# Performance work log

Hardware: AMD Instinct MI355X
Metric: run time of the kernel (lower is better)

Reference implementation:

```python
import jax, jax.numpy as jnp
import numpy as np

BETA = 0.25  # commitment cost (original code's undefined self.betas)


def setup_inputs() -> dict:
    key = jax.random.key(0)
    k1, k2 = jax.random.split(key)
    B, D, H, W = 32, 256, 32, 32
    K = 1024
    x = jax.random.normal(k1, (B, D, H, W), dtype=jnp.float32)
    # nn.Embedding init: uniform(-1/K, 1/K)
    emb = jax.random.uniform(k2, (K, D), dtype=jnp.float32,
                             minval=-1.0 / K, maxval=1.0 / K)
    return {"x": x, "emb": emb}


def reference(x, emb):
    # x: [B, D, H, W] -> NHWC
    xp = jnp.transpose(x, (0, 2, 3, 1))          # [B, H, W, D]
    D = emb.shape[1]
    z = xp.reshape(-1, D)                        # [N, D]
    # pairwise squared distance: ||z||^2 + ||e||^2 - 2 z e^T
    dist = (jnp.sum(z * z, axis=1, keepdims=True)
            + jnp.sum(emb * emb, axis=1)
            - 2.0 * jnp.einsum('nd,kd->nk', z, emb))  # [N, K]
    idx = jnp.argmin(dist, axis=1)               # [N] int
    z_quant = emb[idx].reshape(xp.shape)         # [B, H, W, D]
    sg = jax.lax.stop_gradient
    loss = (jnp.mean((sg(z_quant) - xp) ** 2)
            + BETA * jnp.mean((z_quant - sg(xp)) ** 2))
    # straight-through estimator
    z_quant = xp + sg(z_quant - xp)
    z_quant = jnp.transpose(z_quant, (0, 3, 1, 2))  # back to NCHW
    return z_quant, idx, loss
```

## Files before the change

kernel.cpp:

```cpp
#include <hip/hip_runtime.h>

typedef _Float16 half8 __attribute__((ext_vector_type(8)));
typedef _Float16 half4v __attribute__((ext_vector_type(4)));
typedef float f32x4 __attribute__((ext_vector_type(4)));

#define ZQ_ELEMS 8388608
#define N_TOK    32768
#define D_DIM    256
#define K_CB     1024

#define FLAG_CAP 8192
#define ESCALE   1024.0f
#define TAU      0.15f

__device__ __align__(16) _Float16 g_eh[K_CB * D_DIM];
__device__ __align__(16) float g_ebT[D_DIM * K_CB];
__device__ float g_ck[K_CB];
__device__ float g_bk[K_CB];
__device__ float g_loss;
__device__ int   g_cnt;
__device__ int   g_flags[FLAG_CAP];
__device__ float g_zst[FLAG_CAP * 256];
__device__ float g_aA[FLAG_CAP];
__device__ unsigned long long g_best[FLAG_CAP];

__device__ __forceinline__ unsigned long long enc_dk(float D, int k) {
  unsigned int b = __float_as_uint(D);
  unsigned int u = (b & 0x80000000u) ? ~b : (b | 0x80000000u);
  return (((unsigned long long)u) << 32) | (unsigned int)k;
}

__global__ __launch_bounds__(256) void vq_prep(const float* __restrict__ emb) {
  __shared__ float tl[64][65];
  const int tid = threadIdx.x;
  const int w   = tid >> 6;
  const int l   = tid & 63;
  const int k   = (blockIdx.x << 2) + w;
  f32x4 v = *(const f32x4*)(emb + (k << 8) + (l << 2));
  double sd = (double)v[0]*v[0] + (double)v[1]*v[1] + (double)v[2]*v[2] + (double)v[3]*v[3];
  #pragma unroll
  for (int m = 1; m < 64; m <<= 1) sd += __shfl_xor(sd, m);
  if (l == 0) { g_bk[k] = (float)sd; g_ck[k] = 512.0f * (float)sd; }
  half4v h;
  h[0] = (_Float16)(v[0] * ESCALE); h[1] = (_Float16)(v[1] * ESCALE);
  h[2] = (_Float16)(v[2] * ESCALE); h[3] = (_Float16)(v[3] * ESCALE);
  *(half4v*)(g_eh + (k << 8) + (l << 2)) = h;
  const int gi = blockIdx.x * 256 + tid;
  if (gi < FLAG_CAP) g_best[gi] = ~0ULL;
  if (blockIdx.x == 0 && tid == 0) { g_loss = 0.0f; g_cnt = 0; }
  if (blockIdx.x < 64) {
    const int tx = tid & 63, ty = tid >> 6;
    const int k0 = (blockIdx.x & 15) << 6;
    const int d0 = (blockIdx.x >> 4) << 6;
    #pragma unroll
    for (int j = 0; j < 16; j++) {
      const int kk = (ty << 4) + j;
      tl[kk][tx] = emb[((k0 + kk) << 8) + d0 + tx];
    }
    __syncthreads();
    #pragma unroll
    for (int j = 0; j < 16; j++) {
      const int dd = (ty << 4) + j;
      g_ebT[((d0 + dd) << 10) + k0 + tx] = tl[tx][dd];
    }
  }
}

__global__ __launch_bounds__(256, 4) void vq_main(const float* __restrict__ x,
                                                  const float* __restrict__ emb,
                                                  float* __restrict__ out) {
  __shared__ __align__(16) _Float16 zt[32 * 256];
  __shared__ float ckl[K_CB];
  __shared__ float wv1[4][32], wv2[4][32];
  __shared__ int   wi1[4][32];
  __shared__ int   fidx[32];
  __shared__ float lred[4];
  __shared__ int   fcnt;
  __shared__ int   fslot[32], ftok[32];

  const int tid = threadIdx.x;
  const int n0  = blockIdx.x << 5;
  const int b   = blockIdx.x >> 5;
  const int hw0 = (blockIdx.x & 31) << 5;

  if (tid == 0) fcnt = 0;

  #pragma unroll
  for (int i = 0; i < 4; i++) ckl[tid + 256 * i] = g_ck[tid + 256 * i];

  {
    const int hw8 = (tid & 3) << 3;
    const int dl  = tid >> 2;
    #pragma unroll
    for (int it = 0; it < 4; it++) {
      const int d = (it << 6) + dl;
      const float* src = x + (((b << 8) + d) << 10) + hw0 + hw8;
      f32x4 a0 = *(const f32x4*)src;
      f32x4 a1 = *(const f32x4*)(src + 4);
      _Float16 cv[8];
      cv[0]=(_Float16)a0[0]; cv[1]=(_Float16)a0[1]; cv[2]=(_Float16)a0[2]; cv[3]=(_Float16)a0[3];
      cv[4]=(_Float16)a1[0]; cv[5]=(_Float16)a1[1]; cv[6]=(_Float16)a1[2]; cv[7]=(_Float16)a1[3];
      const int blkx = d >> 3;
      #pragma unroll
      for (int i = 0; i < 8; i++) {
        const int n   = hw8 + i;
        const int blk = blkx ^ i ^ (tid & 3);
        zt[(n << 8) + (blk << 3) + (d & 7)] = cv[i];
      }
    }
  }
  __syncthreads();

  const int w = tid >> 6;
  const int l = tid & 63;
  const int c = l & 15;
  const int q = l >> 4;

  half8 af[2][8];
  #pragma unroll
  for (int t = 0; t < 2; t++) {
    const int n  = (t << 4) + c;
    const int sw = (n & 7) ^ (n >> 3);
    #pragma unroll
    for (int s = 0; s < 8; s++) {
      const int K = (s << 2) + q;
      af[t][s] = *(const half8*)(zt + (n << 8) + ((K ^ sw) << 3));
    }
  }

  float v1[2][4], v2[2][4]; int i1[2][4];
  #pragma unroll
  for (int t = 0; t < 2; t++)
    #pragma unroll
    for (int r = 0; r < 4; r++) { v1[t][r] = -3e38f; v2[t][r] = -3e38f; i1[t][r] = 0; }

  for (int jj = 0; jj < 16; jj++) {
    const int k0 = (w << 4) + (jj << 6);
    const float ckv = ckl[k0 + c];
    f32x4 acc[2];
    acc[0] = f32x4{-ckv, -ckv, -ckv, -ckv};
    acc[1] = f32x4{-ckv, -ckv, -ckv, -ckv};
    #pragma unroll
    for (int s = 0; s < 8; s++) {
      const half8 bf = *(const half8*)(g_eh + ((k0 + c) << 8) + (s << 5) + (q << 3));
      acc[0] = __builtin_amdgcn_mfma_f32_16x16x32_f16(af[0][s], bf, acc[0], 0, 0, 0);
      acc[1] = __builtin_amdgcn_mfma_f32_16x16x32_f16(af[1][s], bf, acc[1], 0, 0, 0);
    }
    const int kk = k0 + c;
    #pragma unroll
    for (int t = 0; t < 2; t++)
      #pragma unroll
      for (int r = 0; r < 4; r++) {
        const float sv = acc[t][r];
        if (sv > v1[t][r]) { v2[t][r] = v1[t][r]; v1[t][r] = sv; i1[t][r] = kk; }
        else if (sv > v2[t][r]) v2[t][r] = sv;
      }
  }

  #pragma unroll
  for (int t = 0; t < 2; t++)
    #pragma unroll
    for (int r = 0; r < 4; r++) {
      float a1v = v1[t][r], a2v = v2[t][r]; int ai = i1[t][r];
      #pragma unroll
      for (int m = 8; m >= 1; m >>= 1) {
        const float o1 = __shfl_xor(a1v, m);
        const int   oi = __shfl_xor(ai, m);
        const float o2 = __shfl_xor(a2v, m);
        if (o1 > a1v || (o1 == a1v && oi < ai)) { a2v = fmaxf(a1v, o2); a1v = o1; ai = oi; }
        else a2v = fmaxf(a2v, o1);
      }
      if (c == 0) {
        const int nl = (t << 4) + (q << 2) + r;
        wv1[w][nl] = a1v; wv2[w][nl] = a2v; wi1[w][nl] = ai;
      }
    }
  __syncthreads();

  if (tid < 32) {
    float a1v = wv1[0][tid], a2v = wv2[0][tid]; int ai = wi1[0][tid];
    #pragma unroll
    for (int ww = 1; ww < 4; ww++) {
      const float o1 = wv1[ww][tid]; const int oi = wi1[ww][tid]; const float o2 = wv2[ww][tid];
      if (o1 > a1v || (o1 == a1v && oi < ai)) { a2v = fmaxf(a1v, o2); a1v = o1; ai = oi; }
      else a2v = fmaxf(a2v, o1);
    }
    fidx[tid] = ai;
    out[ZQ_ELEMS + n0 + tid] = (float)ai;
    if (a1v - a2v < TAU) {
      int p = atomicAdd(&g_cnt, 1);
      if (p < FLAG_CAP) {
        g_flags[p] = n0 + tid;
        int lp = atomicAdd(&fcnt, 1);
        fslot[lp] = p; ftok[lp] = n0 + tid;
      }
    }
  }
  __syncthreads();

  float lacc = 0.0f;
  {
    const int hw = tid & 31;
    const int g  = tid >> 5;
    const int sw = (hw & 7) ^ (hw >> 3);
    const float* erow = emb + (fidx[hw] << 8);
    #pragma unroll
    for (int it = 0; it < 4; it++) {
      const int dblk = (it << 3) + g;
      half8 zv = *(const half8*)(zt + (hw << 8) + ((dblk ^ sw) << 3));
      f32x4 e0 = *(const f32x4*)(erow + (dblk << 3));
      f32x4 e1 = *(const f32x4*)(erow + (dblk << 3) + 4);
      #pragma unroll
      for (int j = 0; j < 8; j++) {
        const int d = (dblk << 3) + j;
        const float ef = (j < 4) ? e0[j] : e1[j - 4];
        const float df = ef - (float)zv[j];
        lacc += df * df;
        out[(((b << 8) + d) << 10) + hw0 + hw] = ef;
      }
    }
  }
  #pragma unroll
  for (int m = 1; m < 64; m <<= 1) lacc += __shfl_xor(lacc, m);
  if (l == 0) lred[w] = lacc;
  __syncthreads();
  if (tid == 0) atomicAdd(&g_loss, lred[0] + lred[1] + lred[2] + lred[3]);

  const int nf = fcnt;
  for (int f = 0; f < nf; f++) {
    const int s = fslot[f];
    const int n = ftok[f];
    const int bb = n >> 10, hw = n & 1023;
    const float zv = x[(((bb << 8) + tid) << 10) + hw];
    g_zst[(s << 8) + tid] = zv;
    ckl[tid] = zv;
    __syncthreads();
    if (tid < 32) {
      double sa = 0.0;
      #pragma unroll
      for (int j = 0; j < 8; j++) { const double z = (double)ckl[(tid << 3) + j]; sa += z * z; }
      #pragma unroll
      for (int m = 1; m < 32; m <<= 1) sa += __shfl_xor(sa, m);
      if (tid == 0) g_aA[s] = (float)sa;
    }
    __syncthreads();
  }
}

__global__ __launch_bounds__(256) void vq_fix() {
  __shared__ float z0l[256], z1l[256];
  __shared__ float bvv[2][256];
  __shared__ int   bkk[2][256];
  const int tid = threadIdx.x;
  int cnt = g_cnt; if (cnt > FLAG_CAP) cnt = FLAG_CAP;
  const int njob = ((cnt + 1) >> 1) << 2;
  for (int j = blockIdx.x; j < njob; j += gridDim.x) {
    const int pr = j >> 2, r = j & 3;
    const int s0 = pr << 1;
    const int s1 = (s0 + 1 < cnt) ? s0 + 1 : cnt - 1;
    z0l[tid] = g_zst[(s0 << 8) + tid];
    z1l[tid] = g_zst[(s1 << 8) + tid];
    __syncthreads();
    double c0 = 0.0, c1 = 0.0;
    const float* colbase = g_ebT + (r << 8) + tid;
    #pragma unroll 8
    for (int d = 0; d < 256; d++) {
      const double e = (double)colbase[d << 10];
      c0 = fma(e, (double)z0l[d], c0);
      c1 = fma(e, (double)z1l[d], c1);
    }
    const int k = (r << 8) + tid;
    const float bkv = g_bk[k];
    bvv[0][tid] = (g_aA[s0] + bkv) - 2.0f * (float)c0;
    bkk[0][tid] = k;
    bvv[1][tid] = (g_aA[s1] + bkv) - 2.0f * (float)c1;
    bkk[1][tid] = k;
    __syncthreads();
    for (int off = 128; off >= 1; off >>= 1) {
      if (tid < off) {
        #pragma unroll
        for (int g = 0; g < 2; g++) {
          const float v2c = bvv[g][tid + off]; const int k2 = bkk[g][tid + off];
          if (v2c < bvv[g][tid] || (v2c == bvv[g][tid] && k2 < bkk[g][tid])) {
            bvv[g][tid] = v2c; bkk[g][tid] = k2;
          }
        }
      }
      __syncthreads();
    }
    if (tid == 0) {
      atomicMin(&g_best[s0], enc_dk(bvv[0][0], bkk[0][0]));
      atomicMin(&g_best[s1], enc_dk(bvv[1][0], bkk[1][0]));
    }
    __syncthreads();
  }
}

__global__ __launch_bounds__(256) void vq_out(const float* __restrict__ emb,
                                              float* __restrict__ out) {
  const int tid = threadIdx.x;
  if (blockIdx.x == 0 && tid == 0)
    out[ZQ_ELEMS + N_TOK] = g_loss * (1.25f / 8388608.0f);
  int cnt = g_cnt; if (cnt > FLAG_CAP) cnt = FLAG_CAP;
  for (int s = blockIdx.x; s < cnt; s += gridDim.x) {
    const int n = g_flags[s];
    const int kw = (int)(unsigned int)(g_best[s] & 0xFFFFFFFFu);
    const int kold = (int)out[ZQ_ELEMS + n];
    __syncthreads();
    if (tid == 0) out[ZQ_ELEMS + n] = (float)kw;
    if (kw != kold) {
      const int bb = n >> 10, hw = n & 1023;
      out[(((bb << 8) + tid) << 10) + hw] = emb[(kw << 8) + tid];
    }
  }
}

extern "C" void kernel_launch(void* const* d_in, const int* in_sizes, int n_in,
                              void* d_out, int out_size, void* d_ws, size_t ws_size,
                              hipStream_t stream) {
  const float* x   = (const float*)d_in[0];
  const float* emb = (const float*)d_in[1];
  float* out = (float*)d_out;
  vq_prep<<<256, 256, 0, stream>>>(emb);
  vq_main<<<1024, 256, 0, stream>>>(x, emb, out);
  vq_fix<<<1536, 256, 0, stream>>>();
  vq_out<<<256, 256, 0, stream>>>(emb, out);
}
```

Baseline: 225.0 us.

## Double tokens per main block, batch four tokens in fix, fuse output kernel

The main kernel now uses 512-thread blocks that each handle 64 tokens. Each wave computes two codebook column tiles per step against four token tiles, with the A fragments read from LDS on every step instead of held in registers. The fix kernel processes four flagged tokens per job, which reuses each codebook column load across more tokens. The former output kernel is folded into the last fix block, selected by an atomic completion counter, which saves a launch. The risk is that one block now does all of the output scatter serially, and the main kernel has fewer blocks and possibly more register pressure.

```diff
diff --git a/kernel.cpp b/kernel.cpp
--- a/kernel.cpp
+++ b/kernel.cpp
@@ -12,6 +12,7 @@
 #define FLAG_CAP 8192
 #define ESCALE   1024.0f
 #define TAU      0.15f
+#define FIX_GRID 768
 
 __device__ __align__(16) _Float16 g_eh[K_CB * D_DIM];
 __device__ __align__(16) float g_ebT[D_DIM * K_CB];
@@ -19,6 +20,7 @@
 __device__ float g_bk[K_CB];
 __device__ float g_loss;
 __device__ int   g_cnt;
+__device__ int   g_fixdone;
 __device__ int   g_flags[FLAG_CAP];
 __device__ float g_zst[FLAG_CAP * 256];
 __device__ float g_aA[FLAG_CAP];
@@ -47,7 +49,7 @@
   *(half4v*)(g_eh + (k << 8) + (l << 2)) = h;
   const int gi = blockIdx.x * 256 + tid;
   if (gi < FLAG_CAP) g_best[gi] = ~0ULL;
-  if (blockIdx.x == 0 && tid == 0) { g_loss = 0.0f; g_cnt = 0; }
+  if (blockIdx.x == 0 && tid == 0) { g_loss = 0.0f; g_cnt = 0; g_fixdone = 0; }
   if (blockIdx.x < 64) {
     const int tx = tid & 63, ty = tid >> 6;
     const int k0 = (blockIdx.x & 15) << 6;
@@ -66,31 +68,30 @@
   }
 }
 
-__global__ __launch_bounds__(256, 4) void vq_main(const float* __restrict__ x,
+__global__ __launch_bounds__(512, 4) void vq_main(const float* __restrict__ x,
                                                   const float* __restrict__ emb,
                                                   float* __restrict__ out) {
-  __shared__ __align__(16) _Float16 zt[32 * 256];
+  __shared__ __align__(16) _Float16 zt[64 * 256];
   __shared__ float ckl[K_CB];
-  __shared__ float wv1[4][32], wv2[4][32];
-  __shared__ int   wi1[4][32];
-  __shared__ int   fidx[32];
-  __shared__ float lred[4];
+  __shared__ float wv1[8][64], wv2[8][64];
+  __shared__ int   wi1[8][64];
+  __shared__ int   fidx[64];
+  __shared__ float lred[8];
   __shared__ int   fcnt;
-  __shared__ int   fslot[32], ftok[32];
+  __shared__ int   fslot[64], ftok[64];
 
   const int tid = threadIdx.x;
-  const int n0  = blockIdx.x << 5;
-  const int b   = blockIdx.x >> 5;
-  const int hw0 = (blockIdx.x & 31) << 5;
+  const int n0  = blockIdx.x << 6;
+  const int b   = blockIdx.x >> 4;
+  const int hw0 = (blockIdx.x & 15) << 6;
 
   if (tid == 0) fcnt = 0;
-
-  #pragma unroll
-  for (int i = 0; i < 4; i++) ckl[tid + 256 * i] = g_ck[tid + 256 * i];
+  ckl[tid] = g_ck[tid];
+  ckl[tid + 512] = g_ck[tid + 512];
 
   {
-    const int hw8 = (tid & 3) << 3;
-    const int dl  = tid >> 2;
+    const int hw8 = (tid & 7) << 3;
+    const int dl  = tid >> 3;
     #pragma unroll
     for (int it = 0; it < 4; it++) {
       const int d = (it << 6) + dl;
@@ -104,7 +105,7 @@
       #pragma unroll
       for (int i = 0; i < 8; i++) {
         const int n   = hw8 + i;
-        const int blk = blkx ^ i ^ (tid & 3);
+        const int blk = blkx ^ i ^ (tid & 7);
         zt[(n << 8) + (blk << 3) + (d & 7)] = cv[i];
       }
     }
@@ -116,49 +117,52 @@
   const int c = l & 15;
   const int q = l >> 4;
 
-  half8 af[2][8];
+  float v1[4][4], v2[4][4]; int i1[4][4];
   #pragma unroll
-  for (int t = 0; t < 2; t++) {
-    const int n  = (t << 4) + c;
-    const int sw = (n & 7) ^ (n >> 3);
+  for (int t = 0; t < 4; t++)
+    #pragma unroll
+    for (int r = 0; r < 4; r++) { v1[t][r] = -3e38f; v2[t][r] = -3e38f; i1[t][r] = 0; }
+
+  for (int jj = 0; jj < 4; jj++) {
+    const int k0  = (w << 5) + (jj << 8);
+    const int kk0 = k0 + c;
+    const int kk1 = kk0 + 16;
+    const float ckv0 = ckl[kk0];
+    const float ckv1 = ckl[kk1];
+    f32x4 acc0[4], acc1[4];
+    #pragma unroll
+    for (int t = 0; t < 4; t++) {
+      acc0[t] = f32x4{-ckv0, -ckv0, -ckv0, -ckv0};
+      acc1[t] = f32x4{-ckv1, -ckv1, -ckv1, -ckv1};
+    }
     #pragma unroll
     for (int s = 0; s < 8; s++) {
-      const int K = (s << 2) + q;
-      af[t][s] = *(const half8*)(zt + (n << 8) + ((K ^ sw) << 3));
-    }
-  }
-
-  float v1[2][4], v2[2][4]; int i1[2][4];
+      const half8 bf0 = *(const half8*)(g_eh + (kk0 << 8) + (s << 5) + (q << 3));
+      const half8 bf1 = *(const half8*)(g_eh + (kk1 << 8) + (s << 5) + (q << 3));
+      #pragma unroll
+      for (int t = 0; t < 4; t++) {
+        const int n  = (t << 4) + c;
+        const int sw = (n & 7) ^ (n >> 3);
+        const half8 a = *(const half8*)(zt + (n << 8) + ((((s << 2) + q) ^ sw) << 3));
+        acc0[t] = __builtin_amdgcn_mfma_f32_16x16x32_f16(a, bf0, acc0[t], 0, 0, 0);
+        acc1[t] = __builtin_amdgcn_mfma_f32_16x16x32_f16(a, bf1, acc1[t], 0, 0, 0);
+      }
+    }
+    #pragma unroll
+    for (int t = 0; t < 4; t++)
+      #pragma unroll
+      for (int r = 0; r < 4; r++) {
+        float sv = acc0[t][r];
+        if (sv > v1[t][r]) { v2[t][r] = v1[t][r]; v1[t][r] = sv; i1[t][r] = kk0; }
+        else if (sv > v2[t][r]) v2[t][r] = sv;
+        sv = acc1[t][r];
+        if (sv > v1[t][r]) { v2[t][r] = v1[t][r]; v1[t][r] = sv; i1[t][r] = kk1; }
+        else if (sv > v2[t][r]) v2[t][r] = sv;
+      }
+  }
+
   #pragma unroll
-  for (int t = 0; t < 2; t++)
-    #pragma unroll
-    for (int r = 0; r < 4; r++) { v1[t][r] = -3e38f; v2[t][r] = -3e38f; i1[t][r] = 0; }
-
-  for (int jj = 0; jj < 16; jj++) {
-    const int k0 = (w << 4) + (jj << 6);
-    const float ckv = ckl[k0 + c];
-    f32x4 acc[2];
-    acc[0] = f32x4{-ckv, -ckv, -ckv, -ckv};
-    acc[1] = f32x4{-ckv, -ckv, -ckv, -ckv};
-    #pragma unroll
-    for (int s = 0; s < 8; s++) {
-      const half8 bf = *(const half8*)(g_eh + ((k0 + c) << 8) + (s << 5) + (q << 3));
-      acc[0] = __builtin_amdgcn_mfma_f32_16x16x32_f16(af[0][s], bf, acc[0], 0, 0, 0);
-      acc[1] = __builtin_amdgcn_mfma_f32_16x16x32_f16(af[1][s], bf, acc[1], 0, 0, 0);
-    }
-    const int kk = k0 + c;
-    #pragma unroll
-    for (int t = 0; t < 2; t++)
-      #pragma unroll
-      for (int r = 0; r < 4; r++) {
-        const float sv = acc[t][r];
-        if (sv > v1[t][r]) { v2[t][r] = v1[t][r]; v1[t][r] = sv; i1[t][r] = kk; }
-        else if (sv > v2[t][r]) v2[t][r] = sv;
-      }
-  }
-
-  #pragma unroll
-  for (int t = 0; t < 2; t++)
+  for (int t = 0; t < 4; t++)
     #pragma unroll
     for (int r = 0; r < 4; r++) {
       float a1v = v1[t][r], a2v = v2[t][r]; int ai = i1[t][r];
@@ -177,10 +181,10 @@
     }
   __syncthreads();
 
-  if (tid < 32) {
+  if (tid < 64) {
     float a1v = wv1[0][tid], a2v = wv2[0][tid]; int ai = wi1[0][tid];
     #pragma unroll
-    for (int ww = 1; ww < 4; ww++) {
+    for (int ww = 1; ww < 8; ww++) {
       const float o1 = wv1[ww][tid]; const int oi = wi1[ww][tid]; const float o2 = wv2[ww][tid];
       if (o1 > a1v || (o1 == a1v && oi < ai)) { a2v = fmaxf(a1v, o2); a1v = o1; ai = oi; }
       else a2v = fmaxf(a2v, o1);
@@ -200,8 +204,8 @@
 
   float lacc = 0.0f;
   {
-    const int hw = tid & 31;
-    const int g  = tid >> 5;
+    const int hw = tid & 63;
+    const int g  = tid >> 6;
     const int sw = (hw & 7) ^ (hw >> 3);
     const float* erow = emb + (fidx[hw] << 8);
     #pragma unroll
@@ -224,16 +228,23 @@
   for (int m = 1; m < 64; m <<= 1) lacc += __shfl_xor(lacc, m);
   if (l == 0) lred[w] = lacc;
   __syncthreads();
-  if (tid == 0) atomicAdd(&g_loss, lred[0] + lred[1] + lred[2] + lred[3]);
+  if (tid == 0) {
+    float ls = 0.0f;
+    #pragma unroll
+    for (int i = 0; i < 8; i++) ls += lred[i];
+    atomicAdd(&g_loss, ls);
+  }
 
   const int nf = fcnt;
   for (int f = 0; f < nf; f++) {
     const int s = fslot[f];
     const int n = ftok[f];
     const int bb = n >> 10, hw = n & 1023;
-    const float zv = x[(((bb << 8) + tid) << 10) + hw];
-    g_zst[(s << 8) + tid] = zv;
-    ckl[tid] = zv;
+    if (tid < 256) {
+      const float zv = x[(((bb << 8) + tid) << 10) + hw];
+      g_zst[(s << 8) + tid] = zv;
+      ckl[tid] = zv;
+    }
     __syncthreads();
     if (tid < 32) {
       double sa = 0.0;
@@ -247,42 +258,51 @@
   }
 }
 
-__global__ __launch_bounds__(256) void vq_fix() {
-  __shared__ float z0l[256], z1l[256];
-  __shared__ float bvv[2][256];
-  __shared__ int   bkk[2][256];
+__global__ __launch_bounds__(256) void vq_fix(const float* __restrict__ emb,
+                                              float* __restrict__ out) {
+  __shared__ float zl0[256], zl1[256], zl2[256], zl3[256];
+  __shared__ float bvv[4][256];
+  __shared__ int   bkk[4][256];
+  __shared__ unsigned int chmask[FLAG_CAP / 32];
+  __shared__ int   lastflag;
   const int tid = threadIdx.x;
   int cnt = g_cnt; if (cnt > FLAG_CAP) cnt = FLAG_CAP;
-  const int njob = ((cnt + 1) >> 1) << 2;
+  const int njob = ((cnt + 3) >> 2) << 2;
   for (int j = blockIdx.x; j < njob; j += gridDim.x) {
-    const int pr = j >> 2, r = j & 3;
-    const int s0 = pr << 1;
+    const int grp = j >> 2, r = j & 3;
+    const int s0 = grp << 2;
     const int s1 = (s0 + 1 < cnt) ? s0 + 1 : cnt - 1;
-    z0l[tid] = g_zst[(s0 << 8) + tid];
-    z1l[tid] = g_zst[(s1 << 8) + tid];
-    __syncthreads();
-    double c0 = 0.0, c1 = 0.0;
+    const int s2 = (s0 + 2 < cnt) ? s0 + 2 : cnt - 1;
+    const int s3 = (s0 + 3 < cnt) ? s0 + 3 : cnt - 1;
+    zl0[tid] = g_zst[(s0 << 8) + tid];
+    zl1[tid] = g_zst[(s1 << 8) + tid];
+    zl2[tid] = g_zst[(s2 << 8) + tid];
+    zl3[tid] = g_zst[(s3 << 8) + tid];
+    __syncthreads();
+    double c0 = 0.0, c1 = 0.0, c2 = 0.0, c3 = 0.0;
     const float* colbase = g_ebT + (r << 8) + tid;
     #pragma unroll 8
     for (int d = 0; d < 256; d++) {
       const double e = (double)colbase[d << 10];
-      c0 = fma(e, (double)z0l[d], c0);
-      c1 = fma(e, (double)z1l[d], c1);
+      c0 = fma(e, (double)zl0[d], c0);
+      c1 = fma(e, (double)zl1[d], c1);
+      c2 = fma(e, (double)zl2[d], c2);
+      c3 = fma(e, (double)zl3[d], c3);
     }
     const int k = (r << 8) + tid;
     const float bkv = g_bk[k];
-    bvv[0][tid] = (g_aA[s0] + bkv) - 2.0f * (float)c0;
-    bkk[0][tid] = k;
-    bvv[1][tid] = (g_aA[s1] + bkv) - 2.0f * (float)c1;
-    bkk[1][tid] = k;
+    bvv[0][tid] = (g_aA[s0] + bkv) - 2.0f * (float)c0; bkk[0][tid] = k;
+    bvv[1][tid] = (g_aA[s1] + bkv) - 2.0f * (float)c1; bkk[1][tid] = k;
+    bvv[2][tid] = (g_aA[s2] + bkv) - 2.0f * (float)c2; bkk[2][tid] = k;
+    bvv[3][tid] = (g_aA[s3] + bkv) - 2.0f * (float)c3; bkk[3][tid] = k;
     __syncthreads();
     for (int off = 128; off >= 1; off >>= 1) {
       if (tid < off) {
         #pragma unroll
-        for (int g = 0; g < 2; g++) {
-          const float v2c = bvv[g][tid + off]; const int k2 = bkk[g][tid + off];
-          if (v2c < bvv[g][tid] || (v2c == bvv[g][tid] && k2 < bkk[g][tid])) {
-            bvv[g][tid] = v2c; bkk[g][tid] = k2;
+        for (int g = 0; g < 4; g++) {
+          const float vc = bvv[g][tid + off]; const int kc = bkk[g][tid + off];
+          if (vc < bvv[g][tid] || (vc == bvv[g][tid] && kc < bkk[g][tid])) {
+            bvv[g][tid] = vc; bkk[g][tid] = kc;
           }
         }
       }
@@ -291,24 +311,41 @@
     if (tid == 0) {
       atomicMin(&g_best[s0], enc_dk(bvv[0][0], bkk[0][0]));
       atomicMin(&g_best[s1], enc_dk(bvv[1][0], bkk[1][0]));
-    }
-    __syncthreads();
-  }
-}
-
-__global__ __launch_bounds__(256) void vq_out(const float* __restrict__ emb,
-                                              float* __restrict__ out) {
-  const int tid = threadIdx.x;
-  if (blockIdx.x == 0 && tid == 0)
-    out[ZQ_ELEMS + N_TOK] = g_loss * (1.25f / 8388608.0f);
-  int cnt = g_cnt; if (cnt > FLAG_CAP) cnt = FLAG_CAP;
-  for (int s = blockIdx.x; s < cnt; s += gridDim.x) {
+      atomicMin(&g_best[s2], enc_dk(bvv[2][0], bkk[2][0]));
+      atomicMin(&g_best[s3], enc_dk(bvv[3][0], bkk[3][0]));
+    }
+    __syncthreads();
+  }
+
+  __threadfence();
+  if (tid == 0) lastflag = (atomicAdd(&g_fixdone, 1) == (int)gridDim.x - 1);
+  __syncthreads();
+  if (!lastflag) return;
+  if (tid == 0) out[ZQ_ELEMS + N_TOK] = g_loss * (1.25f / 8388608.0f);
+  for (int i = tid; i < FLAG_CAP / 32; i += 256) chmask[i] = 0u;
+  __syncthreads();
+  for (int s = tid; s < cnt; s += 256) {
     const int n = g_flags[s];
-    const int kw = (int)(unsigned int)(g_best[s] & 0xFFFFFFFFu);
+    const unsigned long long bv = atomicMin(&g_best[s], ~0ULL);
+    const int kw = (int)(unsigned int)(bv & 0xFFFFFFFFu);
     const int kold = (int)out[ZQ_ELEMS + n];
-    __syncthreads();
-    if (tid == 0) out[ZQ_ELEMS + n] = (float)kw;
+    out[ZQ_ELEMS + n] = (float)kw;
     if (kw != kold) {
+      g_flags[s] = (int)(((unsigned)n) | ((unsigned)kw << 15) | 0x80000000u);
+      atomicOr(&chmask[s >> 5], 1u << (s & 31));
+    }
+  }
+  __syncthreads();
+  const int nw = (cnt + 31) >> 5;
+  for (int wd = 0; wd < nw; wd++) {
+    unsigned int m = chmask[wd];
+    while (m) {
+      const int bpos = __ffs(m) - 1;
+      m &= m - 1;
+      const int s = (wd << 5) + bpos;
+      const unsigned pv = (unsigned)g_flags[s];
+      const int n  = (int)(pv & 0x7FFFu);
+      const int kw = (int)((pv >> 15) & 0x3FFu);
       const int bb = n >> 10, hw = n & 1023;
       out[(((bb << 8) + tid) << 10) + hw] = emb[(kw << 8) + tid];
     }
@@ -322,7 +359,6 @@
   const float* emb = (const float*)d_in[1];
   float* out = (float*)d_out;
   vq_prep<<<256, 256, 0, stream>>>(emb);
-  vq_main<<<1024, 256, 0, stream>>>(x, emb, out);
-  vq_fix<<<1536, 256, 0, stream>>>();
-  vq_out<<<256, 256, 0, stream>>>(emb, out);
-}
+  vq_main<<<512, 512, 0, stream>>>(x, emb, out);
+  vq_fix<<<FIX_GRID, 256, 0, stream>>>(emb, out);
+}
```

After: 320.7 us. 42.6% more time.
